# Kernel tuning notes

Measured on AMD Instinct MI355X. Metric: run time of the kernel, lower is better.

Reference implementation:

```python
import jax, jax.numpy as jnp
import numpy as np
import itertools
from itertools import combinations

N_QUBITS = 6
DIM = 2 ** N_QUBITS            # 64
N_GEN = DIM ** 2 - 1           # 4095 (SU(2^n) generators)
K_LOCAL = 2
OBS_DIM = 2 ** K_LOCAL         # 4
WIRE_GROUPS = [list(c) for c in combinations(range(N_QUBITS), K_LOCAL)]
N_OBS = len(WIRE_GROUPS)       # 15
N_OFF = OBS_DIM * (OBS_DIM - 1) // 2  # 6
CHUNK_DIM = 512
T_EMB = 256
HID = 256
BATCH = 512

# lower-triangle (i>j) flat ordering used by create_Hermitian: c = i*(i-1)/2 + j
_TRI_R = np.array([i for i in range(1, OBS_DIM) for j in range(i)])
_TRI_C = np.array([j for i in range(1, OBS_DIM) for j in range(i)])
_DIAG = np.arange(OBS_DIM - 1)  # diag slots 0..N-2 get 2*D[1..N-1]; last diag is 0


def _pauli_basis():
    """Lexicographic Pauli words on N_QUBITS qubits, identity excluded -> (N_GEN, DIM, DIM)."""
    I = np.eye(2, dtype=np.complex64)
    X = np.array([[0, 1], [1, 0]], dtype=np.complex64)
    Y = np.array([[0, -1j], [1j, 0]], dtype=np.complex64)
    Z = np.array([[1, 0], [0, -1]], dtype=np.complex64)
    P1 = {'I': I, 'X': X, 'Y': Y, 'Z': Z}
    out = np.empty((N_GEN, DIM, DIM), dtype=np.complex64)
    k = 0
    for word in itertools.product('IXYZ', repeat=N_QUBITS):
        if all(c == 'I' for c in word):
            continue
        m = np.array([[1.0 + 0j]], dtype=np.complex64)
        for c in word:
            m = np.kron(m, P1[c])
        out[k] = m
        k += 1
    return jnp.asarray(out)


def setup_inputs() -> dict:
    key = jax.random.key(0)
    ks = jax.random.split(key, 12)
    inp = {
        'x': jax.random.normal(ks[0], (BATCH, CHUNK_DIM + T_EMB), dtype=jnp.float32),
        # enc_proj: Linear(768,256) -> SiLU -> Linear(256,4095)
        'W1': jax.random.normal(ks[1], (CHUNK_DIM + T_EMB, HID), dtype=jnp.float32) * 0.02,
        'b1': jnp.zeros((HID,), dtype=jnp.float32),
        'W2': jax.random.normal(ks[2], (HID, N_GEN), dtype=jnp.float32) * 0.02,
        'b2': jnp.zeros((N_GEN,), dtype=jnp.float32),
        # ANO Hermitian params (std=2.0 per torch init)
        'Aoff': jax.random.normal(ks[3], (N_OBS, N_OFF), dtype=jnp.float32) * 2.0,
        'Boff': jax.random.normal(ks[4], (N_OBS, N_OFF), dtype=jnp.float32) * 2.0,
        'Ddiag': jax.random.normal(ks[5], (N_OBS, OBS_DIM), dtype=jnp.float32) * 2.0,
        # vel_head: Linear(15,256) -> SiLU -> Linear(256,512)
        'Wv1': jax.random.normal(ks[6], (N_OBS, HID), dtype=jnp.float32) * 0.02,
        'bv1': jnp.zeros((HID,), dtype=jnp.float32),
        'Wv2': jax.random.normal(ks[7], (HID, CHUNK_DIM), dtype=jnp.float32) * 0.02,
        'bv2': jnp.zeros((CHUNK_DIM,), dtype=jnp.float32),
        'pauli': _pauli_basis(),  # fixed SU(2^n) generator basis (constant)
    }
    return inp


def _build_H(Aoff, Boff, Ddiag):
    """Batched create_Hermitian: (N_OBS, 4, 4) complex. h + h^H semantics."""
    H = jnp.zeros((N_OBS, OBS_DIM, OBS_DIM), dtype=jnp.complex64)
    off = Aoff.astype(jnp.complex64) + 1j * Boff.astype(jnp.complex64)
    H = H.at[:, _TRI_R, _TRI_C].set(off)
    H = H + jnp.conj(jnp.swapaxes(H, -1, -2))
    H = H.at[:, _DIAG, _DIAG].set((2.0 * Ddiag[:, 1:]).astype(jnp.complex64))
    return H


def _forward(x, W1, b1, W2, b2, Aoff, Boff, Ddiag, Wv1, bv1, Wv2, bv2, pauli):
    B = x.shape[0]
    # enc_proj MLP -> SU(2^n) angles theta (B, 4095)
    enc = jax.nn.silu(x @ W1 + b1) @ W2 + b2
    # SpecialUnitary: U = exp(i * sum_m theta_m P_m); apply to |0...0> via eigh of the
    # Hermitian effective generator H_eff = sum_m theta_m P_m.
    H_eff = jnp.einsum('bm,mij->bij', enc.astype(jnp.complex64), pauli)  # (B, 64, 64)
    lam, V = jnp.linalg.eigh(H_eff)
    # psi = V @ diag(exp(i*lam)) @ V^dag @ e0 ; (V^dag e0)_j = conj(V[0, j])
    psi = jnp.einsum('bij,bj->bi', V, jnp.exp(1j * lam.astype(jnp.complex64)) * jnp.conj(V[:, 0, :]))
    H = _build_H(Aoff, Boff, Ddiag)  # (15, 4, 4)
    psi_t = psi.reshape((B,) + (2,) * N_QUBITS)
    q = []
    for w, (a, b) in enumerate(WIRE_GROUPS):
        # bring wires (a,b) to front (wire order: first wire is most significant bit)
        pg = jnp.moveaxis(psi_t, (1 + a, 1 + b), (1, 2)).reshape(B, OBS_DIM, -1)
        # <H> = tr(rho H), rho_kl = sum_r psi[k,r] conj(psi[l,r])
        q.append(jnp.einsum('bkr,blr,lk->b', pg, jnp.conj(pg), H[w]).real)
    q = jnp.stack(q, axis=1).astype(jnp.float32)  # (B, 15)
    return jax.nn.silu(q @ Wv1 + bv1) @ Wv2 + bv2  # (B, 512)


def reference(x, W1, b1, W2, b2, Aoff, Boff, Ddiag, Wv1, bv1, Wv2, bv2, pauli):
    return _forward(x, W1, b1, W2, b2, Aoff, Boff, Ddiag, Wv1, bv1, Wv2, bv2, pauli)
```

## Files before the change

### kernel.cpp

```cpp
#include <hip/hip_runtime.h>
#include <hip/hip_bf16.h>

#define BATCH   512
#define INDIM   768
#define HID     256
#define NGEN    4095
#define NGENP   4096
#define NOBS    15
#define OUTDIM  512
#define DIM     64

typedef __hip_bfloat16 bf16;

__device__ int      g_isf32;
__device__ float    g_theta[(size_t)BATCH*NGENP];
__device__ float    g_h[(size_t)BATCH*HID];
__device__ float    g_W2p[(size_t)HID*NGENP];
__device__ float    g_b2p[NGENP];

__device__ __forceinline__ float tof(bf16 v){ return __bfloat162float(v); }
__device__ __forceinline__ float silu(float x){ return x / (1.f + __expf(-x)); }
__device__ __forceinline__ float blo(unsigned u){ return __uint_as_float(u<<16); }
__device__ __forceinline__ float bhi(unsigned u){ return __uint_as_float(u & 0xFFFF0000u); }

template<bool F32>
__device__ __forceinline__ float LD(const void* p, size_t i){
  if(F32) return ((const float*)p)[i];
  else    return tof(((const bf16*)p)[i]);
}

__device__ __forceinline__ unsigned spread6(unsigned x){
  return (x&1u) | ((x&2u)<<1) | ((x&4u)<<2) | ((x&8u)<<3) | ((x&16u)<<4) | ((x&32u)<<5);
}

__device__ __forceinline__ bool detect_f32(const unsigned* __restrict__ w1raw, int* red){
  const int t = threadIdx.x & (blockDim.x-1);
  const int lane = t & 63, wav = t >> 6;
  int c = 0;
  for(int i=t;i<1024;i+=(int)blockDim.x){
    unsigned ub = (w1raw[i]>>8) & 0x7Fu;
    if(ub>=0x30u && ub<=0x3Fu) c++;
  }
  #pragma unroll
  for(int s=1;s<64;s<<=1) c += __shfl_xor(c, s);
  if(lane==0) red[wav] = c;
  __syncthreads();
  int nw = (int)blockDim.x >> 6;
  int tot = 0;
  for(int w=0;w<nw;w++) tot += red[w];
  return tot < 512;
}

__constant__ int c_WA[15] = {0,0,0,0,0,1,1,1,1,2,2,2,3,3,4};
__constant__ int c_WB[15] = {1,2,3,4,5,2,3,4,5,3,4,5,4,5,5};
__constant__ int c_Lt[6]  = {1,2,2,3,3,3};
__constant__ int c_Kt[6]  = {0,0,1,0,1,2};

template<bool F32>
__device__ void pack_body(const void* __restrict__ W2, const void* __restrict__ b2){
  const size_t gid = (size_t)blockIdx.x*256 + threadIdx.x;
  const size_t stride = (size_t)gridDim.x*256;
  for(size_t i=gid;i<(size_t)HID*NGENP;i+=stride){
    size_t k = i>>12, c = i&4095;
    g_W2p[i] = (c<NGEN) ? LD<F32>(W2,k*NGEN+c) : 0.f;
  }
  for(size_t i=gid;i<NGENP;i+=stride) g_b2p[i] = (i<NGEN) ? LD<F32>(b2,i) : 0.f;
}

__global__ __launch_bounds__(256) void k_pack(const void* W1,const void* W2,const void* b2){
  __shared__ int red[4];
  bool isf32 = detect_f32((const unsigned*)W1, red);
  if(blockIdx.x==0 && threadIdx.x==0) g_isf32 = isf32 ? 1 : 0;
  if(isf32) pack_body<true >(W2,b2);
  else      pack_body<false>(W2,b2);
}

template<bool F32>
__device__ void enc1_body(const void* __restrict__ x, const void* __restrict__ W1,
                          const void* __restrict__ b1, float* xl){
  const int b = blockIdx.x, t = threadIdx.x;
  for(int k=t;k<INDIM;k+=256) xl[k] = LD<F32>(x,(size_t)b*INDIM+k);
  __syncthreads();
  float acc = 0.f;
  float wA[8], wB[8];
  #pragma unroll
  for(int u=0;u<8;u++) wA[u] = LD<F32>(W1,(size_t)u*HID+t);
  for(int k0=0;k0<INDIM;k0+=16){
    #pragma unroll
    for(int u=0;u<8;u++) wB[u] = LD<F32>(W1,(size_t)(k0+8+u)*HID+t);
    #pragma unroll
    for(int u=0;u<8;u++) acc += xl[k0+u]*wA[u];
    if(k0+16<INDIM){
      #pragma unroll
      for(int u=0;u<8;u++) wA[u] = LD<F32>(W1,(size_t)(k0+16+u)*HID+t);
    }
    #pragma unroll
    for(int u=0;u<8;u++) acc += xl[k0+8+u]*wB[u];
  }
  g_h[(size_t)b*HID+t] = silu(acc + LD<F32>(b1,t));
}

__global__ __launch_bounds__(256) void k_enc1(const void* x,const void* W1,const void* b1){
  __shared__ __align__(16) float xl[INDIM];
  if(g_isf32) enc1_body<true >(x,W1,b1,xl);
  else        enc1_body<false>(x,W1,b1,xl);
}

__global__ __launch_bounds__(256) void k_enc2(){
  __shared__ __align__(16) float hl[HID][8];
  const int t  = threadIdx.x;
  const int b0 = (blockIdx.x>>2)*8;
  const int c0 = (blockIdx.x&3)*1024;
  for(int i=t;i<8*HID;i+=256){
    int r = i>>8, k = i&255;
    hl[k][r] = g_h[(size_t)(b0+r)*HID + k];
  }
  __syncthreads();
  const int col = c0 + 4*t;
  const float* Wbase = g_W2p + col;
  float4 bv = *(const float4*)&g_b2p[col];
  float acc[8][4];
  #pragma unroll
  for(int r=0;r<8;r++){ acc[r][0]=bv.x; acc[r][1]=bv.y; acc[r][2]=bv.z; acc[r][3]=bv.w; }

  float4 wA[8], wB[8];
  #pragma unroll
  for(int u=0;u<8;u++) wA[u] = *(const float4*)&Wbase[(size_t)u*NGENP];

  for(int k0=0;k0<HID;k0+=16){
    #pragma unroll
    for(int u=0;u<8;u++) wB[u] = *(const float4*)&Wbase[(size_t)(k0+8+u)*NGENP];
    #pragma unroll
    for(int u=0;u<8;u++){
      float4 wv = wA[u];
      float4 h0 = *(const float4*)&hl[k0+u][0];
      float4 h1 = *(const float4*)&hl[k0+u][4];
      acc[0][0]+=h0.x*wv.x; acc[0][1]+=h0.x*wv.y; acc[0][2]+=h0.x*wv.z; acc[0][3]+=h0.x*wv.w;
      acc[1][0]+=h0.y*wv.x; acc[1][1]+=h0.y*wv.y; acc[1][2]+=h0.y*wv.z; acc[1][3]+=h0.y*wv.w;
      acc[2][0]+=h0.z*wv.x; acc[2][1]+=h0.z*wv.y; acc[2][2]+=h0.z*wv.z; acc[2][3]+=h0.z*wv.w;
      acc[3][0]+=h0.w*wv.x; acc[3][1]+=h0.w*wv.y; acc[3][2]+=h0.w*wv.z; acc[3][3]+=h0.w*wv.w;
      acc[4][0]+=h1.x*wv.x; acc[4][1]+=h1.x*wv.y; acc[4][2]+=h1.x*wv.z; acc[4][3]+=h1.x*wv.w;
      acc[5][0]+=h1.y*wv.x; acc[5][1]+=h1.y*wv.y; acc[5][2]+=h1.y*wv.z; acc[5][3]+=h1.y*wv.w;
      acc[6][0]+=h1.z*wv.x; acc[6][1]+=h1.z*wv.y; acc[6][2]+=h1.z*wv.z; acc[6][3]+=h1.z*wv.w;
      acc[7][0]+=h1.w*wv.x; acc[7][1]+=h1.w*wv.y; acc[7][2]+=h1.w*wv.z; acc[7][3]+=h1.w*wv.w;
    }
    if(k0+16 < HID){
      #pragma unroll
      for(int u=0;u<8;u++) wA[u] = *(const float4*)&Wbase[(size_t)(k0+16+u)*NGENP];
    }
    #pragma unroll
    for(int u=0;u<8;u++){
      float4 wv = wB[u];
      float4 h0 = *(const float4*)&hl[k0+8+u][0];
      float4 h1 = *(const float4*)&hl[k0+8+u][4];
      acc[0][0]+=h0.x*wv.x; acc[0][1]+=h0.x*wv.y; acc[0][2]+=h0.x*wv.z; acc[0][3]+=h0.x*wv.w;
      acc[1][0]+=h0.y*wv.x; acc[1][1]+=h0.y*wv.y; acc[1][2]+=h0.y*wv.z; acc[1][3]+=h0.y*wv.w;
      acc[2][0]+=h0.z*wv.x; acc[2][1]+=h0.z*wv.y; acc[2][2]+=h0.z*wv.z; acc[2][3]+=h0.z*wv.w;
      acc[3][0]+=h0.w*wv.x; acc[3][1]+=h0.w*wv.y; acc[3][2]+=h0.w*wv.z; acc[3][3]+=h0.w*wv.w;
      acc[4][0]+=h1.x*wv.x; acc[4][1]+=h1.x*wv.y; acc[4][2]+=h1.x*wv.z; acc[4][3]+=h1.x*wv.w;
      acc[5][0]+=h1.y*wv.x; acc[5][1]+=h1.y*wv.y; acc[5][2]+=h1.y*wv.z; acc[5][3]+=h1.y*wv.w;
      acc[6][0]+=h1.z*wv.x; acc[6][1]+=h1.z*wv.y; acc[6][2]+=h1.z*wv.z; acc[6][3]+=h1.z*wv.w;
      acc[7][0]+=h1.w*wv.x; acc[7][1]+=h1.w*wv.y; acc[7][2]+=h1.w*wv.z; acc[7][3]+=h1.w*wv.w;
    }
  }
  #pragma unroll
  for(int r=0;r<8;r++){
    float4 o = make_float4(acc[r][0],acc[r][1],acc[r][2],acc[r][3]);
    *(float4*)&g_theta[(size_t)(b0+r)*NGENP + col] = o;
  }
}

template<bool F32>
__device__ void state_body(const void* __restrict__ Aoff, const void* __restrict__ Boff,
                           const void* __restrict__ Ddiag,
                           const void* __restrict__ Wv1, const void* __restrict__ bv1,
                           const void* __restrict__ Wv2, const void* __restrict__ bv2,
                           void* __restrict__ out, char* sm){
  float*  th   = (float*)sm;
  float*  HH   = (float*)(sm + 16384);
  typedef float2 rep_t[66];
  rep_t*  vrA  = (rep_t*)sm;
  rep_t*  vrB  = (rep_t*)(sm + 2112);
  float2* ps   = (float2*)(sm + 4224);
  float2* coef = (float2*)(sm + 4736);
  float*  rs   = (float*)(sm + 6016);
  float*  qacc = (float*)(sm + 6272);
  float*  s_inva = (float*)(sm + 6336);
  int*    s_K    = (int*)(sm + 6340);
  float*  hl   = (float*)(sm + 6400);
  float (*part)[64][8] = (float(*)[64][8])(sm + 7424);
  float*  s2p  = (float*)(sm + 15616);

  const int b = blockIdx.x, t = threadIdx.x;
  float s2l = 0.f;
  for(int m=t;m<NGEN;m+=256){
    float v = g_theta[(size_t)b*NGENP+m];
    th[m] = v;
    s2l += v*v;
  }
  __syncthreads();

  const int lane = t & 63, wav = t >> 6;
  for(int it=0; it<16; ++it){
    int d = (it<<2) | wav;
    unsigned td = (unsigned)(lane & d);
    unsigned tn = (unsigned)(lane & ~d) & 63u;
    unsigned w  = spread6((unsigned)d) + spread6(td) + 3u*spread6(tn);
    float thv = (w==0u) ? 0.f : th[w-1u];
    int ny = __popc(td) & 3;
    float gr = (ny==0)?  thv : (ny==2 ? -thv : 0.f);
    float gi = (ny==1)? -thv : (ny==3 ?  thv : 0.f);
    #pragma unroll
    for(int s=1;s<64;s<<=1){
      float pr = __shfl_xor(gr, s);
      float pi = __shfl_xor(gi, s);
      if(lane & s){ gr = pr - gr; gi = pi - gi; }
      else        { gr = gr + pr; gi = gi + pi; }
    }
    int j = lane ^ d;
    HH[lane*132 + 2*j]   = gr;
    HH[lane*132 + 2*j+1] = gi;
  }
  __syncthreads();

  const int i = t >> 2, c = t & 3, j0 = c*16;
  float hreg[32];
  float rsum = 0.f;
  #pragma unroll
  for(int jj=0;jj<16;jj+=2){
    float4 hv = *(const float4*)&HH[i*132 + 2*(j0+jj)];
    hreg[2*jj+0]=hv.x; hreg[2*jj+1]=hv.y; hreg[2*jj+2]=hv.z; hreg[2*jj+3]=hv.w;
    rsum += fabsf(hv.x)+fabsf(hv.y)+fabsf(hv.z)+fabsf(hv.w);
  }
  rsum += __shfl_xor(rsum,1);
  rsum += __shfl_xor(rsum,2);
  if(c==0) rs[i] = rsum;
  #pragma unroll
  for(int s=1;s<64;s<<=1) s2l += __shfl_xor(s2l, s);
  if(lane==0) s2p[wav] = s2l;
  __syncthreads();

  if(t==0){
    float aG = 0.5f;
    for(int r=0;r<DIM;r++) aG = fmaxf(aG, rs[r]);
    float s2tot = s2p[0]+s2p[1]+s2p[2]+s2p[3];
    float a = fminf(aG, fmaxf(2.3f*sqrtf(s2tot), 0.5f));
    int K = (int)ceilf(a + 4.f*cbrtf(a) + 5.f);
    if(K>150) K=150;
    float bkp=0.f, bk=1e-35f, snorm=0.f;
    for(int k=K+12;k>=1;--k){
      float bkm = (2.f*(float)k/a)*bk - bkp;
      int n = k-1;
      if(n<=K) coef[n].x = bkm;
      if((n&1)==0) snorm += (n==0?1.f:2.f)*bkm;
      bkp = bk; bk = bkm;
    }
    float invs = 1.f/snorm;
    for(int n=0;n<=K;n++){
      float cv = coef[n].x*invs*(n==0?1.f:2.f);
      int p = n&3;
      float cr = (p==0)? cv : (p==2 ? -cv : 0.f);
      float ci = (p==1)? cv : (p==3 ? -cv : 0.f);
      coef[n] = make_float2(cr,ci);
    }
    *s_K = K;
    *s_inva = 1.f/a;
  }
  __syncthreads();
  const float inva = *s_inva;
  const int K = *s_K;

  rep_t* v0r = vrA;
  rep_t* v1r = vrB;
  if(t < DIM){
    float2 w1 = make_float2(HH[t*132+0]*inva, HH[t*132+1]*inva);
    float2 e0 = make_float2(t==0?1.f:0.f, 0.f);
    #pragma unroll
    for(int cc=0;cc<4;cc++){ v0r[cc][t] = e0; v1r[cc][t] = w1; }
    float2 c0 = coef[0], c1 = coef[1];
    float2 p;
    p.x = (t==0?c0.x:0.f) + c1.x*w1.x - c1.y*w1.y;
    p.y = (t==0?c0.y:0.f) + c1.x*w1.y + c1.y*w1.x;
    ps[t] = p;
  }
  __syncthreads();

  for(int k=2;k<=K;k++){
    const float* vb = (const float*)&v1r[c][0];
    float yr=0.f, yi=0.f;
    #pragma unroll
    for(int jj=0;jj<16;jj+=2){
      float4 xv = *(const float4*)&vb[2*(j0+jj)];
      float hr0=hreg[2*jj], hi0=hreg[2*jj+1], hr1=hreg[2*jj+2], hi1=hreg[2*jj+3];
      yr += hr0*xv.x - hi0*xv.y;
      yi += hr0*xv.y + hi0*xv.x;
      yr += hr1*xv.z - hi1*xv.w;
      yi += hr1*xv.w + hi1*xv.z;
    }
    yr += __shfl_xor(yr,1); yr += __shfl_xor(yr,2);
    yi += __shfl_xor(yi,1); yi += __shfl_xor(yi,2);
    if(c==0){
      float2 vm = v0r[0][i];
      float2 vn = make_float2(2.f*inva*yr - vm.x, 2.f*inva*yi - vm.y);
      #pragma unroll
      for(int cc=0;cc<4;cc++) v0r[cc][i] = vn;
      float2 ck = coef[k];
      float2 p = ps[i];
      p.x += ck.x*vn.x - ck.y*vn.y;
      p.y += ck.x*vn.y + ck.y*vn.x;
      ps[i] = p;
    }
    __syncthreads();
    rep_t* tmp = v0r; v0r = v1r; v1r = tmp;
  }

  if(t<NOBS) qacc[t]=0.f;
  __syncthreads();

  if(t<150){
    int w = t/10, s = t%10;
    int posA = 5 - c_WA[w], posB = 5 - c_WB[w];
    float contrib = 0.f;
    bool have = false;
    if(s<4){
      int kk = s;
      if(kk<3){
        float val = 0.f;
        for(int r=0;r<16;r++){
          int idx = (((kk>>1)&1)<<posA) | ((kk&1)<<posB);
          int rb = 3;
          #pragma unroll
          for(int p=5;p>=0;--p){
            if(p==posA || p==posB) continue;
            idx |= ((r>>rb)&1)<<p;
            rb--;
          }
          float2 pv = ps[idx];
          val += pv.x*pv.x + pv.y*pv.y;
        }
        contrib = val*2.f*LD<F32>(Ddiag, w*4 + kk + 1);
        have = true;
      }
    } else {
      int cc = s-4;
      int l = c_Lt[cc], kk = c_Kt[cc];
      float zr=0.f, zi=0.f;
      for(int r=0;r<16;r++){
        int idxk = (((kk>>1)&1)<<posA) | ((kk&1)<<posB);
        int idxl = (((l >>1)&1)<<posA) | ((l &1)<<posB);
        int rb = 3;
        #pragma unroll
        for(int p=5;p>=0;--p){
          if(p==posA || p==posB) continue;
          int bit = (r>>rb)&1;
          idxk |= bit<<p; idxl |= bit<<p;
          rb--;
        }
        float2 pk = ps[idxk], pl = ps[idxl];
        zr += pk.x*pl.x + pk.y*pl.y;
        zi += pk.y*pl.x - pk.x*pl.y;
      }
      contrib = 2.f*(zr*LD<F32>(Aoff,w*6+cc) - zi*LD<F32>(Boff,w*6+cc));
      have = true;
    }
    if(have) atomicAdd(&qacc[w], contrib);
  }
  __syncthreads();

  if(!F32){
    {
      float acc = tof(((const bf16*)bv1)[t]);
      #pragma unroll
      for(int k=0;k<NOBS;k++) acc += qacc[k]*tof(((const bf16*)Wv1)[k*HID+t]);
      hl[t] = silu(acc);
    }
    __syncthreads();
    const int rg = t >> 6;
    const uint4* w2v = (const uint4*)Wv2;
    float a8[8] = {0.f,0.f,0.f,0.f,0.f,0.f,0.f,0.f};
    for(int kk=0; kk<64; kk+=8){
      uint4 wv[8];
      #pragma unroll
      for(int u=0;u<8;u++) wv[u] = w2v[(size_t)(rg*64+kk+u)*64 + lane];
      #pragma unroll
      for(int u=0;u<8;u++){
        float hk = hl[rg*64+kk+u];
        a8[0] += hk*blo(wv[u].x); a8[1] += hk*bhi(wv[u].x);
        a8[2] += hk*blo(wv[u].y); a8[3] += hk*bhi(wv[u].y);
        a8[4] += hk*blo(wv[u].z); a8[5] += hk*bhi(wv[u].z);
        a8[6] += hk*blo(wv[u].w); a8[7] += hk*bhi(wv[u].w);
      }
    }
    #pragma unroll
    for(int j=0;j<8;j++) part[rg][lane][j] = a8[j];
    __syncthreads();
    {
      int cA = 2*t, cB = 2*t+1;
      float vA = tof(((const bf16*)bv2)[cA]);
      float vB = tof(((const bf16*)bv2)[cB]);
      #pragma unroll
      for(int r2=0;r2<4;r2++){
        vA += part[r2][cA>>3][cA&7];
        vB += part[r2][cB>>3][cB&7];
      }
      bf16 ha = __float2bfloat16(vA), hb = __float2bfloat16(vB);
      unsigned pw = (unsigned)(*(unsigned short*)&ha) |
                    ((unsigned)(*(unsigned short*)&hb)<<16);
      ((unsigned*)out)[(size_t)b*(OUTDIM/2) + t] = pw;
    }
  } else {
    {
      float acc = ((const float*)bv1)[t];
      #pragma unroll
      for(int k=0;k<NOBS;k++) acc += qacc[k]*((const float*)Wv1)[k*HID+t];
      hl[t] = silu(acc);
    }
    __syncthreads();
    #pragma unroll
    for(int oo=0;oo<2;oo++){
      int o = t + oo*256;
      float s0=0.f;
      for(int k=0;k<HID;k++) s0 += hl[k]*((const float*)Wv2)[(size_t)k*OUTDIM+o];
      ((float*)out)[(size_t)b*OUTDIM+o] = ((const float*)bv2)[o] + s0;
    }
  }
}

__global__ __launch_bounds__(256) void k_state(const void* Aoff,const void* Boff,const void* Dd,
                                               const void* Wv1,const void* bv1,
                                               const void* Wv2,const void* bv2, void* out){
  __shared__ __align__(16) char sm[50176];
  if(g_isf32) state_body<true >(Aoff,Boff,Dd,Wv1,bv1,Wv2,bv2,out,sm);
  else        state_body<false>(Aoff,Boff,Dd,Wv1,bv1,Wv2,bv2,out,sm);
}

extern "C" void kernel_launch(void* const* d_in, const int* in_sizes, int n_in,
                              void* d_out, int out_size, void* d_ws, size_t ws_size,
                              hipStream_t stream){
  const void* x    = d_in[0];
  const void* W1   = d_in[1];
  const void* b1   = d_in[2];
  const void* W2   = d_in[3];
  const void* b2   = d_in[4];
  const void* Aoff = d_in[5];
  const void* Boff = d_in[6];
  const void* Dd   = d_in[7];
  const void* Wv1  = d_in[8];
  const void* bv1  = d_in[9];
  const void* Wv2  = d_in[10];
  const void* bv2  = d_in[11];

  k_pack <<<1024,256,0,stream>>>(W1,W2,b2);
  k_enc1 <<<BATCH,256,0,stream>>>(x,W1,b1);
  k_enc2 <<<256,256,0,stream>>>();
  k_state<<<BATCH,256,0,stream>>>(Aoff,Boff,Dd,Wv1,bv1,Wv2,bv2,d_out);
}
```

Before: 227.3 us.

## Double k_state threads to 512 and split Chebyshev matvec across eight lanes per row

The state kernel now runs 512 threads per block. Each row of the 64x64 effective Hamiltonian is handled by 8 lanes of 8 columns each instead of 4 lanes of 16, which shortens the serial dot product in each Chebyshev step. Every lane keeps its own replica of the recurrence vectors and partial sums, so the single-lane update and its broadcast writes are removed. The cost is a larger shared-memory layout, an extra shuffle level, idle threads in the output stage, and more threads per block, which may reduce how many blocks fit per CU.

```diff
diff --git a/kernel.cpp b/kernel.cpp
--- a/kernel.cpp
+++ b/kernel.cpp
@@ -177,23 +177,23 @@
                            const void* __restrict__ Wv2, const void* __restrict__ bv2,
                            void* __restrict__ out, char* sm){
   float*  th   = (float*)sm;
-  float*  HH   = (float*)(sm + 16384);
   typedef float2 rep_t[66];
   rep_t*  vrA  = (rep_t*)sm;
-  rep_t*  vrB  = (rep_t*)(sm + 2112);
-  float2* ps   = (float2*)(sm + 4224);
-  float2* coef = (float2*)(sm + 4736);
-  float*  rs   = (float*)(sm + 6016);
-  float*  qacc = (float*)(sm + 6272);
-  float*  s_inva = (float*)(sm + 6336);
-  int*    s_K    = (int*)(sm + 6340);
-  float*  hl   = (float*)(sm + 6400);
-  float (*part)[64][8] = (float(*)[64][8])(sm + 7424);
-  float*  s2p  = (float*)(sm + 15616);
+  rep_t*  vrB  = (rep_t*)(sm + 4224);
+  float2 (*ps4)[66] = (float2(*)[66])(sm + 8448);
+  float2* coef = (float2*)(sm + 12672);
+  float*  rs   = (float*)(sm + 13888);
+  float*  qacc = (float*)(sm + 14144);
+  float*  s_inva = (float*)(sm + 14208);
+  int*    s_K    = (int*)(sm + 14212);
+  float*  s2p  = (float*)(sm + 14224);
+  float*  HH   = (float*)(sm + 16384);
+  float*  hl   = (float*)(sm + 16384);
+  float (*part)[64][8] = (float(*)[64][8])(sm + 17408);
 
   const int b = blockIdx.x, t = threadIdx.x;
   float s2l = 0.f;
-  for(int m=t;m<NGEN;m+=256){
+  for(int m=t;m<NGEN;m+=512){
     float v = g_theta[(size_t)b*NGENP+m];
     th[m] = v;
     s2l += v*v;
@@ -201,8 +201,8 @@
   __syncthreads();
 
   const int lane = t & 63, wav = t >> 6;
-  for(int it=0; it<16; ++it){
-    int d = (it<<2) | wav;
+  for(int it=0; it<8; ++it){
+    int d = (it<<3) | wav;
     unsigned td = (unsigned)(lane & d);
     unsigned tn = (unsigned)(lane & ~d) & 63u;
     unsigned w  = spread6((unsigned)d) + spread6(td) + 3u*spread6(tn);
@@ -223,17 +223,18 @@
   }
   __syncthreads();
 
-  const int i = t >> 2, c = t & 3, j0 = c*16;
-  float hreg[32];
+  const int i = t >> 3, c = t & 7, j0 = c*8;
+  float hreg[16];
   float rsum = 0.f;
   #pragma unroll
-  for(int jj=0;jj<16;jj+=2){
+  for(int jj=0;jj<8;jj+=2){
     float4 hv = *(const float4*)&HH[i*132 + 2*(j0+jj)];
     hreg[2*jj+0]=hv.x; hreg[2*jj+1]=hv.y; hreg[2*jj+2]=hv.z; hreg[2*jj+3]=hv.w;
     rsum += fabsf(hv.x)+fabsf(hv.y)+fabsf(hv.z)+fabsf(hv.w);
   }
   rsum += __shfl_xor(rsum,1);
   rsum += __shfl_xor(rsum,2);
+  rsum += __shfl_xor(rsum,4);
   if(c==0) rs[i] = rsum;
   #pragma unroll
   for(int s=1;s<64;s<<=1) s2l += __shfl_xor(s2l, s);
@@ -243,7 +244,8 @@
   if(t==0){
     float aG = 0.5f;
     for(int r=0;r<DIM;r++) aG = fmaxf(aG, rs[r]);
-    float s2tot = s2p[0]+s2p[1]+s2p[2]+s2p[3];
+    float s2tot = 0.f;
+    for(int w2=0;w2<8;w2++) s2tot += s2p[w2];
     float a = fminf(aG, fmaxf(2.3f*sqrtf(s2tot), 0.5f));
     int K = (int)ceilf(a + 4.f*cbrtf(a) + 5.f);
     if(K>150) K=150;
@@ -272,16 +274,16 @@
 
   rep_t* v0r = vrA;
   rep_t* v1r = vrB;
-  if(t < DIM){
-    float2 w1 = make_float2(HH[t*132+0]*inva, HH[t*132+1]*inva);
-    float2 e0 = make_float2(t==0?1.f:0.f, 0.f);
-    #pragma unroll
-    for(int cc=0;cc<4;cc++){ v0r[cc][t] = e0; v1r[cc][t] = w1; }
+  {
+    float2 w1 = make_float2(HH[i*132+0]*inva, HH[i*132+1]*inva);
+    float2 e0 = make_float2(i==0?1.f:0.f, 0.f);
+    v0r[c][i] = e0;
+    v1r[c][i] = w1;
     float2 c0 = coef[0], c1 = coef[1];
     float2 p;
-    p.x = (t==0?c0.x:0.f) + c1.x*w1.x - c1.y*w1.y;
-    p.y = (t==0?c0.y:0.f) + c1.x*w1.y + c1.y*w1.x;
-    ps[t] = p;
+    p.x = (i==0?c0.x:0.f) + c1.x*w1.x - c1.y*w1.y;
+    p.y = (i==0?c0.y:0.f) + c1.x*w1.y + c1.y*w1.x;
+    ps4[c][i] = p;
   }
   __syncthreads();
 
@@ -289,7 +291,7 @@
     const float* vb = (const float*)&v1r[c][0];
     float yr=0.f, yi=0.f;
     #pragma unroll
-    for(int jj=0;jj<16;jj+=2){
+    for(int jj=0;jj<8;jj+=2){
       float4 xv = *(const float4*)&vb[2*(j0+jj)];
       float hr0=hreg[2*jj], hi0=hreg[2*jj+1], hr1=hreg[2*jj+2], hi1=hreg[2*jj+3];
       yr += hr0*xv.x - hi0*xv.y;
@@ -297,23 +299,21 @@
       yr += hr1*xv.z - hi1*xv.w;
       yi += hr1*xv.w + hi1*xv.z;
     }
-    yr += __shfl_xor(yr,1); yr += __shfl_xor(yr,2);
-    yi += __shfl_xor(yi,1); yi += __shfl_xor(yi,2);
-    if(c==0){
-      float2 vm = v0r[0][i];
-      float2 vn = make_float2(2.f*inva*yr - vm.x, 2.f*inva*yi - vm.y);
-      #pragma unroll
-      for(int cc=0;cc<4;cc++) v0r[cc][i] = vn;
-      float2 ck = coef[k];
-      float2 p = ps[i];
-      p.x += ck.x*vn.x - ck.y*vn.y;
-      p.y += ck.x*vn.y + ck.y*vn.x;
-      ps[i] = p;
-    }
+    yr += __shfl_xor(yr,1); yr += __shfl_xor(yr,2); yr += __shfl_xor(yr,4);
+    yi += __shfl_xor(yi,1); yi += __shfl_xor(yi,2); yi += __shfl_xor(yi,4);
+    float2 vm = v0r[c][i];
+    float2 vn = make_float2(2.f*inva*yr - vm.x, 2.f*inva*yi - vm.y);
+    v0r[c][i] = vn;
+    float2 ck = coef[k];
+    float2 p = ps4[c][i];
+    p.x += ck.x*vn.x - ck.y*vn.y;
+    p.y += ck.x*vn.y + ck.y*vn.x;
+    ps4[c][i] = p;
     __syncthreads();
     rep_t* tmp = v0r; v0r = v1r; v1r = tmp;
   }
 
+  const float2* ps = &ps4[0][0];
   if(t<NOBS) qacc[t]=0.f;
   __syncthreads();
 
@@ -368,33 +368,35 @@
   __syncthreads();
 
   if(!F32){
-    {
+    if(t<HID){
       float acc = tof(((const bf16*)bv1)[t]);
       #pragma unroll
       for(int k=0;k<NOBS;k++) acc += qacc[k]*tof(((const bf16*)Wv1)[k*HID+t]);
       hl[t] = silu(acc);
     }
     __syncthreads();
-    const int rg = t >> 6;
-    const uint4* w2v = (const uint4*)Wv2;
-    float a8[8] = {0.f,0.f,0.f,0.f,0.f,0.f,0.f,0.f};
-    for(int kk=0; kk<64; kk+=8){
-      uint4 wv[8];
-      #pragma unroll
-      for(int u=0;u<8;u++) wv[u] = w2v[(size_t)(rg*64+kk+u)*64 + lane];
-      #pragma unroll
-      for(int u=0;u<8;u++){
-        float hk = hl[rg*64+kk+u];
-        a8[0] += hk*blo(wv[u].x); a8[1] += hk*bhi(wv[u].x);
-        a8[2] += hk*blo(wv[u].y); a8[3] += hk*bhi(wv[u].y);
-        a8[4] += hk*blo(wv[u].z); a8[5] += hk*bhi(wv[u].z);
-        a8[6] += hk*blo(wv[u].w); a8[7] += hk*bhi(wv[u].w);
+    if(t<256){
+      const int rg = t >> 6;
+      const uint4* w2v = (const uint4*)Wv2;
+      float a8[8] = {0.f,0.f,0.f,0.f,0.f,0.f,0.f,0.f};
+      for(int kk=0; kk<64; kk+=8){
+        uint4 wv[8];
+        #pragma unroll
+        for(int u=0;u<8;u++) wv[u] = w2v[(size_t)(rg*64+kk+u)*64 + lane];
+        #pragma unroll
+        for(int u=0;u<8;u++){
+          float hk = hl[rg*64+kk+u];
+          a8[0] += hk*blo(wv[u].x); a8[1] += hk*bhi(wv[u].x);
+          a8[2] += hk*blo(wv[u].y); a8[3] += hk*bhi(wv[u].y);
+          a8[4] += hk*blo(wv[u].z); a8[5] += hk*bhi(wv[u].z);
+          a8[6] += hk*blo(wv[u].w); a8[7] += hk*bhi(wv[u].w);
+        }
       }
-    }
-    #pragma unroll
-    for(int j=0;j<8;j++) part[rg][lane][j] = a8[j];
+      #pragma unroll
+      for(int j=0;j<8;j++) part[rg][lane][j] = a8[j];
+    }
     __syncthreads();
-    {
+    if(t<256){
       int cA = 2*t, cB = 2*t+1;
       float vA = tof(((const bf16*)bv2)[cA]);
       float vB = tof(((const bf16*)bv2)[cB]);
@@ -409,24 +411,26 @@
       ((unsigned*)out)[(size_t)b*(OUTDIM/2) + t] = pw;
     }
   } else {
-    {
+    if(t<HID){
       float acc = ((const float*)bv1)[t];
       #pragma unroll
       for(int k=0;k<NOBS;k++) acc += qacc[k]*((const float*)Wv1)[k*HID+t];
       hl[t] = silu(acc);
     }
     __syncthreads();
-    #pragma unroll
-    for(int oo=0;oo<2;oo++){
-      int o = t + oo*256;
-      float s0=0.f;
-      for(int k=0;k<HID;k++) s0 += hl[k]*((const float*)Wv2)[(size_t)k*OUTDIM+o];
-      ((float*)out)[(size_t)b*OUTDIM+o] = ((const float*)bv2)[o] + s0;
-    }
-  }
-}
-
-__global__ __launch_bounds__(256) void k_state(const void* Aoff,const void* Boff,const void* Dd,
+    if(t<256){
+      #pragma unroll
+      for(int oo=0;oo<2;oo++){
+        int o = t + oo*256;
+        float s0=0.f;
+        for(int k=0;k<HID;k++) s0 += hl[k]*((const float*)Wv2)[(size_t)k*OUTDIM+o];
+        ((float*)out)[(size_t)b*OUTDIM+o] = ((const float*)bv2)[o] + s0;
+      }
+    }
+  }
+}
+
+__global__ __launch_bounds__(512) void k_state(const void* Aoff,const void* Boff,const void* Dd,
                                                const void* Wv1,const void* bv1,
                                                const void* Wv2,const void* bv2, void* out){
   __shared__ __align__(16) char sm[50176];
@@ -453,5 +457,5 @@
   k_pack <<<1024,256,0,stream>>>(W1,W2,b2);
   k_enc1 <<<BATCH,256,0,stream>>>(x,W1,b1);
   k_enc2 <<<256,256,0,stream>>>();
-  k_state<<<BATCH,256,0,stream>>>(Aoff,Boff,Dd,Wv1,bv1,Wv2,bv2,d_out);
-}
+  k_state<<<BATCH,512,0,stream>>>(Aoff,Boff,Dd,Wv1,bv1,Wv2,bv2,d_out);
+}
```

Measured after the change: 229.5 us. Within noise of the previous version (+1.0%).
